# Kernel optimization log

Hardware: AMD Instinct MI355X
Metric: run time of the kernel (lower is better)

Reference implementation:

```python
import jax, jax.numpy as jnp
import numpy as np

B, T, D, H, KH, HD, F, L, V = 2, 2048, 1024, 16, 4, 64, 4096, 4, 32000
G = H // KH  # num_key_value_groups
EPS = 1e-6
SCALE = HD ** -0.5


def setup_inputs() -> dict:
    key = jax.random.key(0)
    ks = jax.random.split(key, 8)
    std = 0.02
    return {
        "input_ids": jax.random.randint(ks[0], (B, T), 0, V, dtype=jnp.int32),
        "embed_w": jax.random.normal(ks[1], (V, D), jnp.float32) * std,
        "pos_w": jax.random.normal(ks[2], (T, D), jnp.float32) * std,
        "ln1_w": jnp.ones((L, D), jnp.float32),
        "ln2_w": jnp.ones((L, D), jnp.float32),
        "wq": jax.random.normal(ks[3], (L, D, H * HD), jnp.float32) * std,
        "wkv": jax.random.normal(ks[4], (L, D, 2 * KH * HD), jnp.float32) * std,
        "wo": jax.random.normal(ks[5], (L, H * HD, D), jnp.float32) * std,
        "w1": jax.random.normal(ks[6], (L, D, F), jnp.float32) * std,
        "w2": jax.random.normal(ks[7], (L, F, D), jnp.float32) * std,
        "norm_w": jnp.ones((D,), jnp.float32),
    }


def _rmsnorm(x, w):
    return x * jax.lax.rsqrt(jnp.mean(x * x, axis=-1, keepdims=True) + EPS) * w


def reference(input_ids, embed_w, pos_w, ln1_w, ln2_w, wq, wkv, wo, w1, w2, norm_w):
    causal = jnp.tril(jnp.ones((T, T), dtype=bool))  # True = keep
    x = embed_w[input_ids] + pos_w[:T]  # [B,T,D]
    for l in range(L):
        h = _rmsnorm(x, ln1_w[l])
        q = (h @ wq[l]).reshape(B, T, H, HD)
        kv = h @ wkv[l]
        k, v = jnp.split(kv, 2, axis=-1)
        k = jnp.repeat(k.reshape(B, T, KH, HD), G, axis=2)  # GQA repeat_interleave
        v = jnp.repeat(v.reshape(B, T, KH, HD), G, axis=2)
        scores = jnp.einsum("bqhd,bkhd->bhqk", q, k) * SCALE
        scores = jnp.where(causal, scores, -jnp.inf)
        p = jax.nn.softmax(scores, axis=-1)
        o = jnp.einsum("bhqk,bkhd->bqhd", p, v).reshape(B, T, H * HD)
        x = x + o @ wo[l]
        h = _rmsnorm(x, ln2_w[l])
        x = x + jax.nn.gelu(h @ w1[l], approximate=False) @ w2[l]
    x = _rmsnorm(x, norm_w)
    logits = x @ embed_w.T  # tied lm_head
    return logits
```

## Files before the change

### kernel.cpp

```cpp
#include <hip/hip_runtime.h>
#include <hip/hip_bf16.h>

#define DI __device__ __forceinline__

typedef unsigned short u16;
typedef unsigned int u32;
typedef __attribute__((ext_vector_type(8))) short bf16x8;
typedef __attribute__((ext_vector_type(4))) float f32x4;

#define B_   2
#define T_   2048
#define D_   1024
#define H_   16
#define KH_  4
#define HD_  64
#define F_   4096
#define L_   4
#define V_   32000
#define M_   (B_ * T_)
#define QKVN (H_*HD_ + 2*KH_*HD_)

DI u16 f2bf(float f) {
  __hip_bfloat16 h = __float2bfloat16(f);
  return *reinterpret_cast<u16*>(&h);
}

DI float bf2f(u16 b) {
  __hip_bfloat16 h = *reinterpret_cast<__hip_bfloat16*>(&b);
  return __bfloat162float(h);
}

DI void gl_lds16(const void* g, void* l) {
  __builtin_amdgcn_global_load_lds(
      (const __attribute__((address_space(1))) u32*)g,
      (__attribute__((address_space(3))) u32*)l, 16, 0, 0);
}

#define BARRIER() do { asm volatile("" ::: "memory"); __builtin_amdgcn_s_barrier(); asm volatile("" ::: "memory"); } while (0)
#define LGK0()    asm volatile("s_waitcnt lgkmcnt(0)" ::: "memory")
#define VMC(n)    asm volatile("s_waitcnt vmcnt(" #n ")" ::: "memory")
#define PRIO(p)   __builtin_amdgcn_s_setprio(p)

__global__ __launch_bounds__(256) void embed_kernel(const int* __restrict__ ids,
                                                    const float* __restrict__ ew,
                                                    const float* __restrict__ pw,
                                                    float* __restrict__ x) {
  const int row = blockIdx.x;
  const int t = row & (T_ - 1);
  const int id = ids[row];
  float4 e = reinterpret_cast<const float4*>(ew + (size_t)id * D_)[threadIdx.x];
  float4 p = reinterpret_cast<const float4*>(pw + (size_t)t * D_)[threadIdx.x];
  e.x += p.x; e.y += p.y; e.z += p.z; e.w += p.w;
  reinterpret_cast<float4*>(x + (size_t)row * D_)[threadIdx.x] = e;
}

__global__ __launch_bounds__(256) void conv_kernel(const float* __restrict__ W,
                                                   u16* __restrict__ Wb) {
  const size_t i = (size_t)blockIdx.x * 256 + threadIdx.x;
  float4 v = reinterpret_cast<const float4*>(W)[i];
  ushort4 ov;
  ov.x = f2bf(v.x); ov.y = f2bf(v.y); ov.z = f2bf(v.z); ov.w = f2bf(v.w);
  reinterpret_cast<ushort4*>(Wb)[i] = ov;
}

__global__ __launch_bounds__(256) void convt_fused(const float* __restrict__ wq,
                                                   const float* __restrict__ wkv,
                                                   const float* __restrict__ wo,
                                                   const float* __restrict__ w1,
                                                   const float* __restrict__ w2,
                                                   u16* __restrict__ wtq,
                                                   u16* __restrict__ wto,
                                                   u16* __restrict__ wt1,
                                                   u16* __restrict__ wt2) {
  const int t = blockIdx.x;
  const float* W; u16* Wt; int K, N, local;
  if (t < 1024)      { W = wq;  Wt = wtq;               K = 1024; N = 1024; local = t; }
  else if (t < 1536) { W = wkv; Wt = wtq + 1024*1024;   K = 1024; N = 512;  local = t - 1024; }
  else if (t < 2560) { W = wo;  Wt = wto;               K = 1024; N = 1024; local = t - 1536; }
  else if (t < 6656) { W = w1;  Wt = wt1;               K = 1024; N = 4096; local = t - 2560; }
  else               { W = w2;  Wt = wt2;               K = 4096; N = 1024; local = t - 6656; }
  const int nk = K >> 5;
  const int k0 = (local % nk) * 32, n0 = (local / nk) * 32;
  __shared__ float tb[32][33];
  const int tx = threadIdx.x & 31, ty = threadIdx.x >> 5;
  #pragma unroll
  for (int i = 0; i < 4; i++)
    tb[ty + i*8][tx] = W[(size_t)(k0 + ty + i*8) * N + n0 + tx];
  __syncthreads();
  #pragma unroll
  for (int i = 0; i < 4; i++)
    Wt[(size_t)(n0 + ty + i*8) * K + k0 + tx] = f2bf(tb[tx][ty + i*8]);
}

__global__ __launch_bounds__(256) void rmsnorm_kernel(const float* __restrict__ x,
                                                      const float* __restrict__ w,
                                                      u16* __restrict__ out) {
  const int row = blockIdx.x;
  const int tid = threadIdx.x;
  float4 v = reinterpret_cast<const float4*>(x + (size_t)row * D_)[tid];
  float ss = v.x*v.x + v.y*v.y + v.z*v.z + v.w*v.w;
  #pragma unroll
  for (int off = 32; off > 0; off >>= 1) ss += __shfl_down(ss, off, 64);
  __shared__ float red[4];
  if ((tid & 63) == 0) red[tid >> 6] = ss;
  __syncthreads();
  const float tot = red[0] + red[1] + red[2] + red[3];
  const float rstd = rsqrtf(tot * (1.0f / D_) + 1e-6f);
  float4 wv = reinterpret_cast<const float4*>(w)[tid];
  ushort4 ov;
  ov.x = f2bf(v.x * rstd * wv.x);
  ov.y = f2bf(v.y * rstd * wv.y);
  ov.z = f2bf(v.z * rstd * wv.z);
  ov.w = f2bf(v.w * rstd * wv.w);
  reinterpret_cast<ushort4*>(out + (size_t)row * D_)[tid] = ov;
}

template <int EPI>
__global__ __launch_bounds__(256) void gemm_bt(const u16* __restrict__ A,
                                               const u16* __restrict__ Bt,
                                               const float* __restrict__ res,
                                               u16* __restrict__ Cb,
                                               float* __restrict__ Cf,
                                               int M, int N, int K) {
  __shared__ u16 As[128 * 64];
  __shared__ u16 Bs[128 * 64];
  const int tid = threadIdx.x;
  const int n0 = blockIdx.x * 128;
  const int m0 = blockIdx.y * 128;
  const int lane = tid & 63, wave = tid >> 6;
  const int wm = wave >> 1, wn = wave & 1;
  const int l15 = lane & 15, l4 = lane >> 4;
  const int srow = tid >> 3, scol = (tid & 7) * 8;
  const u16* ag = A + (size_t)(m0 + srow) * K + scol;
  const u16* bg = Bt + (size_t)(n0 + srow) * K + scol;
  u16* asd = &As[srow * 64 + scol];
  u16* bsd = &Bs[srow * 64 + scol];
  f32x4 acc[4][4] = {};
  const int nk = K >> 6;
  for (int kt = 0; kt < nk; kt++) {
    const int k0 = kt * 64;
    __syncthreads();
    #pragma unroll
    for (int i = 0; i < 4; i++) gl_lds16(ag + (size_t)i*32*K + k0, asd + i*32*64);
    #pragma unroll
    for (int i = 0; i < 4; i++) gl_lds16(bg + (size_t)i*32*K + k0, bsd + i*32*64);
    __syncthreads();
    #pragma unroll
    for (int s = 0; s < 2; s++) {
      bf16x8 af[4], bfv[4];
      #pragma unroll
      for (int i = 0; i < 4; i++)
        af[i] = *reinterpret_cast<const bf16x8*>(&As[(wm*64 + i*16 + l15)*64 + s*32 + l4*8]);
      #pragma unroll
      for (int j = 0; j < 4; j++)
        bfv[j] = *reinterpret_cast<const bf16x8*>(&Bs[(wn*64 + j*16 + l15)*64 + s*32 + l4*8]);
      #pragma unroll
      for (int i = 0; i < 4; i++)
        #pragma unroll
        for (int j = 0; j < 4; j++)
          acc[i][j] = __builtin_amdgcn_mfma_f32_16x16x32_bf16(bfv[j], af[i], acc[i][j], 0, 0, 0);
    }
  }
  #pragma unroll
  for (int i = 0; i < 4; i++) {
    const int row = m0 + wm*64 + i*16 + l15;
    #pragma unroll
    for (int j = 0; j < 4; j++) {
      const int colb = n0 + wn*64 + j*16 + l4*4;
      const size_t idx = (size_t)row * N + colb;
      const f32x4 v = acc[i][j];
      if (EPI == 0) {
        ushort4 ov;
        ov.x = f2bf(v[0]); ov.y = f2bf(v[1]); ov.z = f2bf(v[2]); ov.w = f2bf(v[3]);
        *reinterpret_cast<ushort4*>(&Cb[idx]) = ov;
      } else {
        const float4 rv = *reinterpret_cast<const float4*>(&res[idx]);
        float4 ov;
        ov.x = v[0] + rv.x; ov.y = v[1] + rv.y; ov.z = v[2] + rv.z; ov.w = v[3] + rv.w;
        *reinterpret_cast<float4*>(&Cf[idx]) = ov;
      }
    }
  }
}

template <int EPI>
__global__ __launch_bounds__(512, 2) void gemm256(const u16* __restrict__ A,
                                                  const u16* __restrict__ Bt,
                                                  u16* __restrict__ Cb,
                                                  float* __restrict__ Cf,
                                                  int M, int N, int K) {
  __shared__ char lds[131072];
  char* const AsB = lds;
  char* const BsB = lds + 65536;
  const int tid = threadIdx.x;
  const int lane = tid & 63, wave = tid >> 6;
  const int wm = wave >> 2, wn = wave & 3;
  const int l15 = lane & 15, l4 = lane >> 4;

  const int nm = M >> 8;
  const int nwg = nm * (N >> 8);
  const int cpx = nwg >> 3;
  const int bid = blockIdx.x;
  const int wg = (bid & 7) * cpx + (bid >> 3);
  const int m0 = (wg % nm) << 8;
  const int n0 = (wg / nm) << 8;

  const u16* const Atile = A + (size_t)m0 * K;
  const u16* const Btile = Bt + (size_t)n0 * K;

  int soff[2][2], pd[2][2];
  #pragma unroll
  for (int h = 0; h < 2; ++h)
    #pragma unroll
    for (int jj = 0; jj < 2; ++jj) {
      const int row = h*128 + jj*64 + (tid >> 3);
      const int sl  = (tid & 7) ^ (row & 7);
      soff[h][jj] = row * K + sl * 8;
      pd[h][jj]   = h*16384 + jj*8192 + tid*16;
    }
  const int swz = (l15 & 7) << 4;
  const int rb0 = l15*128 + ((l4*16)      ^ swz);
  const int rb1 = l15*128 + ((64 + l4*16) ^ swz);

  #define STA(S,H,T) do { const u16* g_ = Atile + (T)*64; char* d_ = AsB + (S)*32768; \
      gl_lds16(g_ + soff[H][0], d_ + pd[H][0]); gl_lds16(g_ + soff[H][1], d_ + pd[H][1]); } while (0)
  #define STB(S,H,T) do { const u16* g_ = Btile + (T)*64; char* d_ = BsB + (S)*32768; \
      gl_lds16(g_ + soff[H][0], d_ + pd[H][0]); gl_lds16(g_ + soff[H][1], d_ + pd[H][1]); } while (0)
  #define RDA(S,GI,RB) (*reinterpret_cast<const bf16x8*>(AsB + (S)*32768 + (GI)*2048 + (RB)))
  #define RDB(S,GJ,RB) (*reinterpret_cast<const bf16x8*>(BsB + (S)*32768 + (GJ)*2048 + (RB)))

  f32x4 acc[8][4] = {};
  bf16x8 Ar[4][2], Br[4][2];

  #define RDA03(S) { _Pragma("unroll") for (int i=0;i<4;++i){ Ar[i][0]=RDA(S,i*2+wm,rb0); Ar[i][1]=RDA(S,i*2+wm,rb1);} }
  #define RDA47(S) { _Pragma("unroll") for (int i=0;i<4;++i){ Ar[i][0]=RDA(S,(i+4)*2+wm,rb0); Ar[i][1]=RDA(S,(i+4)*2+wm,rb1);} }
  #define RDB01(S) { _Pragma("unroll") for (int j=0;j<2;++j){ Br[j][0]=RDB(S,j*4+wn,rb0); Br[j][1]=RDB(S,j*4+wn,rb1);} }
  #define RDB23(S) { _Pragma("unroll") for (int j=2;j<4;++j){ Br[j][0]=RDB(S,j*4+wn,rb0); Br[j][1]=RDB(S,j*4+wn,rb1);} }
  #define MFQ(IO,JL) { _Pragma("unroll") for (int i=0;i<4;++i) _Pragma("unroll") for (int jj=0;jj<2;++jj) { \
      acc[(IO)+i][(JL)+jj] = __builtin_amdgcn_mfma_f32_16x16x32_bf16(Br[(JL)+jj][0], Ar[i][0], acc[(IO)+i][(JL)+jj],0,0,0); \
      acc[(IO)+i][(JL)+jj] = __builtin_amdgcn_mfma_f32_16x16x32_bf16(Br[(JL)+jj][1], Ar[i][1], acc[(IO)+i][(JL)+jj],0,0,0); } }

  STA(0,0,0); STA(0,1,0); STB(0,0,0); STB(0,1,0);
  VMC(4);
  STA(1,0,1); STB(1,0,1); STB(1,1,1);
  VMC(6);
  BARRIER();

  const int niter = K >> 7;
  for (int it = 0; it < niter; ++it) {
    const int t0 = it*2, t1 = t0 + 1;
    const bool pf = (it + 1 < niter);
    RDA03(0); RDB01(0); STA(1,1,t1);
    BARRIER(); LGK0(); PRIO(1); MFQ(0,0); PRIO(0); BARRIER();
    RDB23(0); if (pf) STA(0,0,t0+2);
    BARRIER(); LGK0(); PRIO(1); MFQ(0,2); PRIO(0); BARRIER();
    RDA47(0); if (pf) STB(0,0,t0+2);
    BARRIER(); LGK0(); PRIO(1); MFQ(4,0); PRIO(0); BARRIER();
    if (pf) { STB(0,1,t0+2); VMC(6); } else { VMC(0); }
    BARRIER(); PRIO(1); MFQ(4,2); PRIO(0); BARRIER();
    RDA03(1); RDB01(1); if (pf) STA(0,1,t0+2);
    BARRIER(); LGK0(); PRIO(1); MFQ(0,0); PRIO(0); BARRIER();
    RDB23(1); if (pf) STA(1,0,t1+2);
    BARRIER(); LGK0(); PRIO(1); MFQ(0,2); PRIO(0); BARRIER();
    RDA47(1); if (pf) STB(1,0,t1+2);
    BARRIER(); LGK0(); PRIO(1); MFQ(4,0); PRIO(0); BARRIER();
    if (pf) { STB(1,1,t1+2); VMC(6); }
    BARRIER(); PRIO(1); MFQ(4,2); PRIO(0); BARRIER();
  }

  #pragma unroll
  for (int i = 0; i < 8; ++i) {
    const int row = m0 + (i*2 + wm)*16 + l15;
    #pragma unroll
    for (int j = 0; j < 4; ++j) {
      const int colb = n0 + (j*4 + wn)*16 + l4*4;
      const f32x4 v = acc[i][j];
      if (EPI == 0) {
        *reinterpret_cast<f32x4*>(&Cf[(size_t)row * N + colb]) = v;
      } else {
        ushort4 ov;
        #pragma unroll
        for (int rr = 0; rr < 4; ++rr) {
          const float g = 0.5f * v[rr] * (1.0f + erff(v[rr] * 0.70710678118f));
          ((u16*)&ov)[rr] = f2bf(g);
        }
        *reinterpret_cast<ushort4*>(&Cb[(size_t)row * N + colb]) = ov;
      }
    }
  }
  #undef STA
  #undef STB
  #undef RDA
  #undef RDB
  #undef RDA03
  #undef RDA47
  #undef RDB01
  #undef RDB23
  #undef MFQ
}

__global__ __launch_bounds__(256) void attn_kernel(const u16* __restrict__ qkv,
                                                   u16* __restrict__ o) {
  const int qt = blockIdx.x;
  const int h  = blockIdx.y;
  const int b  = blockIdx.z;
  const int kh = h / (H_ / KH_);
  __shared__ u16 Ks[64 * 64];
  __shared__ u16 Vt[64 * 66];
  __shared__ u16 Pl[4][16 * 72];
  const int tid = threadIdx.x, lane = tid & 63, wave = tid >> 6;
  const int l15 = lane & 15, l4 = lane >> 4;
  const size_t Mrow = (size_t)b * T_;

  bf16x8 qf[2];
  {
    const u16* qp = qkv + (Mrow + qt*64 + wave*16 + l15) * QKVN + h*HD_ + l4*8;
    qf[0] = *reinterpret_cast<const bf16x8*>(qp);
    qf[1] = *reinterpret_cast<const bf16x8*>(qp + 32);
    #pragma unroll
    for (int s = 0; s < 2; s++)
      #pragma unroll
      for (int j = 0; j < 8; j++)
        qf[s][j] = (short)f2bf(bf2f((u16)qf[s][j]) * 0.125f);
  }
  float m_run[4], l_run[4];
  f32x4 oacc[4] = {};
  #pragma unroll
  for (int r = 0; r < 4; r++) { m_run[r] = -1e30f; l_run[r] = 0.0f; }

  const int srow = tid >> 3, scol = (tid & 7) * 8;
  const int vp = (tid >> 3) * 2;
  const int vd = (tid & 7) * 8;
  for (int kt = 0; kt <= qt; kt++) {
    const u16* kg = qkv + (Mrow + kt*64 + srow) * QKVN + D_ + kh*HD_ + scol;
    const u16* vg = qkv + (Mrow + kt*64 + vp) * QKVN + D_ + KH_*HD_ + kh*HD_ + vd;
    __syncthreads();
    gl_lds16(kg, &Ks[srow*64 + scol]);
    gl_lds16(kg + 32*QKVN, &Ks[(srow+32)*64 + scol]);
    {
      bf16x8 v0 = *reinterpret_cast<const bf16x8*>(vg);
      bf16x8 v1 = *reinterpret_cast<const bf16x8*>(vg + QKVN);
      #pragma unroll
      for (int j = 0; j < 8; j++) {
        const u32 pk = (u32)(u16)v0[j] | ((u32)(u16)v1[j] << 16);
        *reinterpret_cast<u32*>(&Vt[(vd + j)*66 + vp]) = pk;
      }
    }
    __syncthreads();

    f32x4 sa[4] = {};
    #pragma unroll
    for (int s = 0; s < 2; s++)
      #pragma unroll
      for (int n = 0; n < 4; n++) {
        bf16x8 kf = *reinterpret_cast<const bf16x8*>(&Ks[(n*16 + l15)*64 + s*32 + l4*8]);
        sa[n] = __builtin_amdgcn_mfma_f32_16x16x32_bf16(qf[s], kf, sa[n], 0, 0, 0);
      }
    if (kt == qt) {
      const int qloc = wave*16 + l4*4;
      #pragma unroll
      for (int n = 0; n < 4; n++) {
        const int kloc = n*16 + l15;
        #pragma unroll
        for (int r = 0; r < 4; r++)
          if (kloc > qloc + r) sa[n][r] = -1e30f;
      }
    }
    float mx[4];
    #pragma unroll
    for (int r = 0; r < 4; r++)
      mx[r] = fmaxf(fmaxf(sa[0][r], sa[1][r]), fmaxf(sa[2][r], sa[3][r]));
    #pragma unroll
    for (int off = 1; off < 16; off <<= 1)
      #pragma unroll
      for (int r = 0; r < 4; r++)
        mx[r] = fmaxf(mx[r], __shfl_xor(mx[r], off, 64));
    float alpha[4], rs[4];
    #pragma unroll
    for (int r = 0; r < 4; r++) {
      const float nm = fmaxf(m_run[r], mx[r]);
      alpha[r] = __expf(m_run[r] - nm);
      m_run[r] = nm;
      rs[r] = 0.0f;
    }
    u16* pw = &Pl[wave][0];
    #pragma unroll
    for (int n = 0; n < 4; n++)
      #pragma unroll
      for (int r = 0; r < 4; r++) {
        const float p = __expf(sa[n][r] - m_run[r]);
        rs[r] += p;
        pw[(l4*4 + r)*72 + n*16 + l15] = f2bf(p);
      }
    #pragma unroll
    for (int off = 1; off < 16; off <<= 1)
      #pragma unroll
      for (int r = 0; r < 4; r++)
        rs[r] += __shfl_xor(rs[r], off, 64);
    #pragma unroll
    for (int r = 0; r < 4; r++) l_run[r] = l_run[r]*alpha[r] + rs[r];
    #pragma unroll
    for (int n = 0; n < 4; n++)
      #pragma unroll
      for (int r = 0; r < 4; r++) oacc[n][r] *= alpha[r];

    asm volatile("s_waitcnt lgkmcnt(0)" ::: "memory");
    #pragma unroll
    for (int s = 0; s < 2; s++) {
      bf16x8 pa = *reinterpret_cast<const bf16x8*>(&Pl[wave][l15*72 + s*32 + l4*8]);
      #pragma unroll
      for (int n = 0; n < 4; n++) {
        bf16x8 vb = *reinterpret_cast<const bf16x8*>(&Vt[(n*16 + l15)*66 + s*32 + l4*8]);
        oacc[n] = __builtin_amdgcn_mfma_f32_16x16x32_bf16(pa, vb, oacc[n], 0, 0, 0);
      }
    }
  }
  #pragma unroll
  for (int n = 0; n < 4; n++)
    #pragma unroll
    for (int r = 0; r < 4; r++) {
      const float ov = oacc[n][r] / l_run[r];
      const size_t row = Mrow + qt*64 + wave*16 + l4*4 + r;
      o[row * (size_t)(H_*HD_) + h*HD_ + n*16 + l15] = f2bf(ov);
    }
}

#define OFF_X     0ull
#define OFF_H     16777216ull
#define OFF_QKV   25165824ull
#define OFF_O     37748736ull
#define OFF_U     46137344ull
#define OFF_WTQ   79691776ull
#define OFF_WTO   82837504ull
#define OFF_WT1   84934656ull
#define OFF_WT2   93323264ull
#define OFF_EBF   101711872ull

extern "C" void kernel_launch(void* const* d_in, const int* in_sizes, int n_in,
                              void* d_out, int out_size, void* d_ws, size_t ws_size,
                              hipStream_t stream) {
  const int*   ids = (const int*)  d_in[0];
  const float* ew  = (const float*)d_in[1];
  const float* pw  = (const float*)d_in[2];
  const float* ln1 = (const float*)d_in[3];
  const float* ln2 = (const float*)d_in[4];
  const float* wq  = (const float*)d_in[5];
  const float* wkv = (const float*)d_in[6];
  const float* wo  = (const float*)d_in[7];
  const float* w1  = (const float*)d_in[8];
  const float* w2  = (const float*)d_in[9];
  const float* nw  = (const float*)d_in[10];
  float* out = (float*)d_out;

  char* ws = (char*)d_ws;
  float* x   = (float*)(ws + OFF_X);
  u16*   h   = (u16*)  (ws + OFF_H);
  u16*   qkv = (u16*)  (ws + OFF_QKV);
  u16*   o   = (u16*)  (ws + OFF_O);
  u16*   u   = (u16*)  (ws + OFF_U);
  u16*   wtq = (u16*)  (ws + OFF_WTQ);
  u16*   wto = (u16*)  (ws + OFF_WTO);
  u16*   wt1 = (u16*)  (ws + OFF_WT1);
  u16*   wt2 = (u16*)  (ws + OFF_WT2);
  u16*   ebf = (u16*)  (ws + OFF_EBF);

  embed_kernel<<<M_, 256, 0, stream>>>(ids, ew, pw, x);
  conv_kernel<<<(V_*D_/4)/256, 256, 0, stream>>>(ew, ebf);

  for (int l = 0; l < L_; l++) {
    convt_fused<<<10752, 256, 0, stream>>>(
        wq  + (size_t)l*D_*(H_*HD_),
        wkv + (size_t)l*D_*(2*KH_*HD_),
        wo  + (size_t)l*(H_*HD_)*D_,
        w1  + (size_t)l*D_*F_,
        w2  + (size_t)l*F_*D_,
        wtq, wto, wt1, wt2);

    rmsnorm_kernel<<<M_, 256, 0, stream>>>(x, ln1 + (size_t)l*D_, h);
    gemm_bt<0><<<dim3(QKVN/128, M_/128), 256, 0, stream>>>(h, wtq, nullptr, qkv, nullptr, M_, QKVN, D_);
    attn_kernel<<<dim3(T_/64, H_, B_), 256, 0, stream>>>(qkv, o);
    gemm_bt<1><<<dim3(D_/128, M_/128), 256, 0, stream>>>(o, wto, x, nullptr, x, M_, D_, H_*HD_);
    rmsnorm_kernel<<<M_, 256, 0, stream>>>(x, ln2 + (size_t)l*D_, h);
    gemm256<1><<<dim3((F_/256)*(M_/256)), 512, 0, stream>>>(h, wt1, u, nullptr, M_, F_, D_);
    gemm_bt<1><<<dim3(D_/128, M_/128), 256, 0, stream>>>(u, wt2, x, nullptr, x, M_, D_, F_);
  }

  rmsnorm_kernel<<<M_, 256, 0, stream>>>(x, nw, h);
  gemm256<0><<<dim3((V_/256)*(M_/256)), 512, 0, stream>>>(h, ebf, nullptr, out, M_, V_, D_);
}
```

Measured before the change: 1.811 ms.

## Double-buffer K tiles and register-prefetch V in causal attention kernel

```diff
diff --git a/kernel.cpp b/kernel.cpp
--- a/kernel.cpp
+++ b/kernel.cpp
@@ -305,9 +305,9 @@
   const int h  = blockIdx.y;
   const int b  = blockIdx.z;
   const int kh = h / (H_ / KH_);
-  __shared__ u16 Ks[64 * 64];
+  __shared__ u16 Ks[2][64 * 64];
   __shared__ u16 Vt[64 * 66];
-  __shared__ u16 Pl[4][16 * 72];
+  __shared__ u16 Pl[4][16 * 68];
   const int tid = threadIdx.x, lane = tid & 63, wave = tid >> 6;
   const int l15 = lane & 15, l4 = lane >> 4;
   const size_t Mrow = (size_t)b * T_;
@@ -331,29 +331,43 @@
   const int srow = tid >> 3, scol = (tid & 7) * 8;
   const int vp = (tid >> 3) * 2;
   const int vd = (tid & 7) * 8;
+  const u16* const kbase = qkv + Mrow * QKVN + D_ + kh*HD_;
+  const u16* const vbase = kbase + KH_*HD_;
+
+  {
+    const u16* kg = kbase + (size_t)srow * QKVN + scol;
+    gl_lds16(kg, &Ks[0][srow*64 + scol]);
+    gl_lds16(kg + 32*QKVN, &Ks[0][(srow+32)*64 + scol]);
+    const u16* vg = vbase + (size_t)vp * QKVN + vd;
+    bf16x8 v0 = *reinterpret_cast<const bf16x8*>(vg);
+    bf16x8 v1 = *reinterpret_cast<const bf16x8*>(vg + QKVN);
+    #pragma unroll
+    for (int j = 0; j < 8; j++) {
+      const u32 pk = (u32)(u16)v0[j] | ((u32)(u16)v1[j] << 16);
+      *reinterpret_cast<u32*>(&Vt[(vd + j)*66 + vp]) = pk;
+    }
+  }
+  __syncthreads();
+
   for (int kt = 0; kt <= qt; kt++) {
-    const u16* kg = qkv + (Mrow + kt*64 + srow) * QKVN + D_ + kh*HD_ + scol;
-    const u16* vg = qkv + (Mrow + kt*64 + vp) * QKVN + D_ + KH_*HD_ + kh*HD_ + vd;
-    __syncthreads();
-    gl_lds16(kg, &Ks[srow*64 + scol]);
-    gl_lds16(kg + 32*QKVN, &Ks[(srow+32)*64 + scol]);
-    {
-      bf16x8 v0 = *reinterpret_cast<const bf16x8*>(vg);
-      bf16x8 v1 = *reinterpret_cast<const bf16x8*>(vg + QKVN);
-      #pragma unroll
-      for (int j = 0; j < 8; j++) {
-        const u32 pk = (u32)(u16)v0[j] | ((u32)(u16)v1[j] << 16);
-        *reinterpret_cast<u32*>(&Vt[(vd + j)*66 + vp]) = pk;
-      }
-    }
-    __syncthreads();
+    const int cur = kt & 1;
+    const bool pf = kt < qt;
+    bf16x8 v0n, v1n;
+    if (pf) {
+      const u16* kg = kbase + (size_t)((kt+1)*64 + srow) * QKVN + scol;
+      gl_lds16(kg, &Ks[1-cur][srow*64 + scol]);
+      gl_lds16(kg + 32*QKVN, &Ks[1-cur][(srow+32)*64 + scol]);
+      const u16* vg = vbase + (size_t)((kt+1)*64 + vp) * QKVN + vd;
+      v0n = *reinterpret_cast<const bf16x8*>(vg);
+      v1n = *reinterpret_cast<const bf16x8*>(vg + QKVN);
+    }
 
     f32x4 sa[4] = {};
     #pragma unroll
     for (int s = 0; s < 2; s++)
       #pragma unroll
       for (int n = 0; n < 4; n++) {
-        bf16x8 kf = *reinterpret_cast<const bf16x8*>(&Ks[(n*16 + l15)*64 + s*32 + l4*8]);
+        bf16x8 kf = *reinterpret_cast<const bf16x8*>(&Ks[cur][(n*16 + l15)*64 + s*32 + l4*8]);
         sa[n] = __builtin_amdgcn_mfma_f32_16x16x32_bf16(qf[s], kf, sa[n], 0, 0, 0);
       }
     if (kt == qt) {
@@ -390,7 +404,7 @@
       for (int r = 0; r < 4; r++) {
         const float p = __expf(sa[n][r] - m_run[r]);
         rs[r] += p;
-        pw[(l4*4 + r)*72 + n*16 + l15] = f2bf(p);
+        pw[(l4*4 + r)*68 + n*16 + l15] = f2bf(p);
       }
     #pragma unroll
     for (int off = 1; off < 16; off <<= 1)
@@ -407,12 +421,21 @@
     asm volatile("s_waitcnt lgkmcnt(0)" ::: "memory");
     #pragma unroll
     for (int s = 0; s < 2; s++) {
-      bf16x8 pa = *reinterpret_cast<const bf16x8*>(&Pl[wave][l15*72 + s*32 + l4*8]);
+      bf16x8 pa = *reinterpret_cast<const bf16x8*>(&Pl[wave][l15*68 + s*32 + l4*8]);
       #pragma unroll
       for (int n = 0; n < 4; n++) {
         bf16x8 vb = *reinterpret_cast<const bf16x8*>(&Vt[(n*16 + l15)*66 + s*32 + l4*8]);
         oacc[n] = __builtin_amdgcn_mfma_f32_16x16x32_bf16(pa, vb, oacc[n], 0, 0, 0);
       }
+    }
+    __syncthreads();
+    if (pf) {
+      #pragma unroll
+      for (int j = 0; j < 8; j++) {
+        const u32 pk = (u32)(u16)v0n[j] | ((u32)(u16)v1n[j] << 16);
+        *reinterpret_cast<u32*>(&Vt[(vd + j)*66 + vp]) = pk;
+      }
+      __syncthreads();
     }
   }
   #pragma unroll
```

After: 1.807 ms. About the same (-0.2%).
